# Kernel tuning notes

Hardware: AMD Instinct MI355X
Metric: run time of the kernel (lower is better)

The kernel has to match this reference:

```python
import jax, jax.numpy as jnp
import numpy as np

B, E, D, NH, NP = 4, 32, 1024, 16, 4
LQ = E * E
DH = D // NH


def layer_norm(x, g, b, eps=1e-6):
    m = x.mean(-1, keepdims=True)
    v = ((x - m) ** 2).mean(-1, keepdims=True)
    return (x - m) / jnp.sqrt(v + eps) * g + b


def get_ref(H, W):
    # matches MSCrossAttnBlock.get_reference_points: centers normalized to [0,1], (x, y) order
    ys, xs = jnp.meshgrid((jnp.arange(H, dtype=jnp.float32) + 0.5) / H,
                          (jnp.arange(W, dtype=jnp.float32) + 0.5) / W, indexing='ij')
    return jnp.stack([xs.ravel(), ys.ravel()], -1)  # (H*W, 2)


def bilinear_sample(value_l, loc, H, W):
    # value_l: (N, nH, H*W, dh); loc: (N, Lq, nH, P, 2) normalized to [0,1]
    # replicates F.grid_sample(align_corners=False, padding_mode='zeros') with grid = 2*loc - 1
    N, Lq, nH, P, _ = loc.shape
    x = loc[..., 0] * W - 0.5
    y = loc[..., 1] * H - 0.5
    x0 = jnp.floor(x)
    y0 = jnp.floor(y)
    wx1 = x - x0
    wy1 = y - y0
    out = 0.0
    for dy, wy in ((0, 1.0 - wy1), (1, wy1)):
        for dx, wx in ((0, 1.0 - wx1), (1, wx1)):
            xi = x0 + dx
            yi = y0 + dy
            valid = (xi >= 0) & (xi < W) & (yi >= 0) & (yi < H)
            idx = (jnp.clip(yi, 0, H - 1) * W + jnp.clip(xi, 0, W - 1)).astype(jnp.int32)
            idx_t = idx.transpose(0, 2, 1, 3).reshape(N, nH, Lq * P)  # (N, nH, Lq*P)
            g = jnp.take_along_axis(value_l, idx_t[..., None], axis=2)  # (N, nH, Lq*P, dh)
            g = g.reshape(N, nH, Lq, P, -1).transpose(0, 2, 1, 3, 4)  # (N, Lq, nH, P, dh)
            w = (wx * wy) * valid.astype(value_l.dtype)
            out = out + g * w[..., None]
    return out


def msdeform(query, ref, inp, shapes, Wv, bv, Wo, bo, Wa, ba, Wp, bp):
    # MSDeformAttn forward (no padding mask)
    N, Lq, d = query.shape
    nL = len(shapes)
    value = (inp @ Wv.T + bv).reshape(N, -1, NH, DH).transpose(0, 2, 1, 3)  # (N, nH, Lin, dh)
    off = (query @ Wo.T + bo).reshape(N, Lq, NH, nL, NP, 2)
    attw = jax.nn.softmax((query @ Wa.T + ba).reshape(N, Lq, NH, nL * NP), axis=-1)
    attw = attw.reshape(N, Lq, NH, nL, NP)
    normalizer = jnp.array([[w, h] for (h, w) in shapes], dtype=query.dtype)  # (nL, 2) = [W, H]
    loc = ref[None, :, None, None, None, :] + off / normalizer[None, None, None, :, None, :]
    out = 0.0
    start = 0
    for l, (H, W) in enumerate(shapes):
        sampled = bilinear_sample(value[:, :, start:start + H * W], loc[:, :, :, l], H, W)
        out = out + (sampled * attw[:, :, :, l, :, None]).sum(3)  # (N, Lq, nH, dh)
        start += H * W
    return out.reshape(N, Lq, d) @ Wp.T + bp


def setup_inputs() -> dict:
    key = jax.random.key(0)
    ks = iter(jax.random.split(key, 64))
    def rnd(shape, scale):
        return jax.random.normal(next(ks), shape, dtype=jnp.float32) * scale
    inp = {}
    for i in range(4):
        inp[f'src{i}'] = rnd((B, LQ, D), 1.0)
    for nm in ('qn', 'fn', 'n1'):
        inp[nm + '_g'] = jnp.ones((D,), jnp.float32)
        inp[nm + '_b'] = jnp.zeros((D,), jnp.float32)
    inp['gamma1'] = rnd((D,), 0.1)
    inp['gamma2'] = rnd((D,), 0.1)
    ws = D ** -0.5
    for pre, nl in (('ca', 4), ('sa', 1)):
        inp[pre + '_vw'] = rnd((D, D), ws)
        inp[pre + '_vb'] = jnp.zeros((D,), jnp.float32)
        inp[pre + '_ow'] = rnd((NH * nl * NP * 2, D), ws)
        inp[pre + '_ob'] = rnd((NH * nl * NP * 2,), 0.1)
        inp[pre + '_aw'] = rnd((NH * nl * NP, D), ws)
        inp[pre + '_ab'] = jnp.zeros((NH * nl * NP,), jnp.float32)
        inp[pre + '_pw'] = rnd((D, D), ws)
        inp[pre + '_pb'] = jnp.zeros((D,), jnp.float32)
    return inp


def reference(src0, src1, src2, src3, qn_g, qn_b, fn_g, fn_b, n1_g, n1_b, gamma1, gamma2,
              ca_vw, ca_vb, ca_ow, ca_ob, ca_aw, ca_ab, ca_pw, ca_pb,
              sa_vw, sa_vb, sa_ow, sa_ob, sa_aw, sa_ab, sa_pw, sa_pb):
    shapes4 = [(E, E)] * 4
    feat = jnp.concatenate([src0, src1, src2, src3], axis=1)  # (B, 4*LQ, D)
    query = src3  # srcs[-1], pos embed is None
    ref = get_ref(E, E)  # (LQ, 2)
    attn = msdeform(layer_norm(query, qn_g, qn_b), ref, layer_norm(feat, fn_g, fn_b),
                    shapes4, ca_vw, ca_vb, ca_ow, ca_ob, ca_aw, ca_ab, ca_pw, ca_pb)
    attn1 = layer_norm(attn, n1_g, n1_b)
    attn2 = msdeform(attn1, ref, attn1, [(E, E)],
                     sa_vw, sa_vb, sa_ow, sa_ob, sa_aw, sa_ab, sa_pw, sa_pb)
    attn = attn + gamma2 * attn2
    return query + gamma1 * attn
```

## Files before the change

### kernel.cpp

```cpp
#include <hip/hip_runtime.h>


#define DEV __device__ __forceinline__

typedef float f32x4 __attribute__((ext_vector_type(4)));
typedef __bf16 bf16x8 __attribute__((ext_vector_type(8)));

DEV unsigned short f2bf(float f) {
  union { float f; unsigned u; } a; a.f = f;
  unsigned r = a.u + 0x7fffu + ((a.u >> 16) & 1u);
  return (unsigned short)(r >> 16);
}
DEV float bf2f(unsigned short h) {
  union { unsigned u; float f; } a; a.u = ((unsigned)h) << 16;
  return a.f;
}

DEV void gld16(const unsigned short* g, unsigned short* l) {
  __builtin_amdgcn_global_load_lds(
      (const __attribute__((address_space(1))) void*)g,
      (__attribute__((address_space(3))) void*)l, 16, 0, 0);
}

struct CvtArgs {
  const float* src[8];
  unsigned short* dst;
  int off4[9];
};

__global__ __launch_bounds__(256) void f2bf_multi(CvtArgs a) {
  int i = blockIdx.x * 256 + threadIdx.x;
  int seg = 0;
  #pragma unroll
  for (int s = 1; s < 8; ++s) seg += (i >= a.off4[s]) ? 1 : 0;
  const float4 v = ((const float4*)a.src[seg])[i - a.off4[seg]];
  unsigned short* o = a.dst + (size_t)i * 4;
  o[0] = f2bf(v.x); o[1] = f2bf(v.y); o[2] = f2bf(v.z); o[3] = f2bf(v.w);
}

DEV void ln_row(const float* __restrict__ xr, const float* __restrict__ g,
                const float* __restrict__ b, unsigned short* __restrict__ op_row) {
  float4 v = ((const float4*)xr)[threadIdx.x];
  float s  = v.x + v.y + v.z + v.w;
  float s2 = v.x*v.x + v.y*v.y + v.z*v.z + v.w*v.w;
  #pragma unroll
  for (int o = 32; o; o >>= 1) { s += __shfl_down(s, o); s2 += __shfl_down(s2, o); }
  __shared__ float red[8];
  int wave = threadIdx.x >> 6, lane = threadIdx.x & 63;
  if (lane == 0) { red[wave] = s; red[4 + wave] = s2; }
  __syncthreads();
  if (threadIdx.x == 0) {
    float ts  = red[0] + red[1] + red[2] + red[3];
    float ts2 = red[4] + red[5] + red[6] + red[7];
    float mean = ts * (1.f / 1024.f);
    float var  = ts2 * (1.f / 1024.f) - mean * mean;
    red[0] = mean; red[1] = rsqrtf(var + 1e-6f);
  }
  __syncthreads();
  float mean = red[0], rstd = red[1];
  float4 gg = ((const float4*)g)[threadIdx.x];
  float4 bb = ((const float4*)b)[threadIdx.x];
  unsigned short* op = op_row + threadIdx.x * 4;
  op[0] = f2bf((v.x - mean) * rstd * gg.x + bb.x);
  op[1] = f2bf((v.y - mean) * rstd * gg.y + bb.y);
  op[2] = f2bf((v.z - mean) * rstd * gg.z + bb.z);
  op[3] = f2bf((v.w - mean) * rstd * gg.w + bb.w);
}

__global__ __launch_bounds__(256) void ln_bf16_kernel(
    const float* __restrict__ x, const float* __restrict__ g,
    const float* __restrict__ b, unsigned short* __restrict__ out) {
  int row = blockIdx.x;
  ln_row(x + (size_t)row * 1024, g, b, out + (size_t)row * 1024);
}

__global__ __launch_bounds__(256) void ln4_kernel(
    const float* __restrict__ s0, const float* __restrict__ s1,
    const float* __restrict__ s2, const float* __restrict__ s3,
    const float* __restrict__ g, const float* __restrict__ b,
    unsigned short* __restrict__ out) {
  int blk = blockIdx.x;
  int l = blk >> 12, inner = blk & 4095;
  const float* srcs[4] = {s0, s1, s2, s3};
  int orow = (inner >> 10) * 4096 + l * 1024 + (inner & 1023);
  ln_row(srcs[l] + (size_t)inner * 1024, g, b, out + (size_t)orow * 1024);
}

struct GemmP {
  const unsigned short* A; const unsigned short* W;
  void* C; void* C1; void* C2;
  const float* b0; const float* b1; const float* b2;
  const float* src3; const float* g1; const float* g2; const float* attnp;
  int M, N, K;
};

template <int BM, int BN, int EPI>
__global__ __launch_bounds__(256) void gemm_glds(GemmP P) {
  constexpr int BK = 32;
  constexpr int WMT = BM / 2, WNT = BN / 2;
  constexpr int MF = WMT / 16, NF = WNT / 16;
  constexpr int AG = BM / 16, BG = BN / 16;
  constexpr int PA = AG / 4, PB = BG / 4;
  __shared__ __align__(16) unsigned short sA[BM * BK];
  __shared__ __align__(16) unsigned short sB[BN * BK];
  const int tid = threadIdx.x;
  const int wave = tid >> 6, lane = tid & 63;
  const int wm = (wave & 1) * WMT, wn = (wave >> 1) * WNT;
  const int m0 = blockIdx.x * BM, n0 = blockIdx.y * BN;
  const int lq = lane >> 4, lm = lane & 15;
  const int r16 = lane >> 2;
  const int cst = lane & 3;
  const int csrc = cst ^ ((r16 >> 1) & 3);
  const int aslot = lq ^ ((lm >> 1) & 3);

  f32x4 acc[MF][NF] = {};

  for (int k0 = 0; k0 < P.K; k0 += BK) {
    __syncthreads();
    #pragma unroll
    for (int p = 0; p < PA; ++p) {
      int g = wave + 4 * p;
      int grow = m0 + g * 16 + r16;
      gld16(P.A + (size_t)grow * P.K + k0 + csrc * 8, sA + g * 512);
    }
    #pragma unroll
    for (int p = 0; p < PB; ++p) {
      int g = wave + 4 * p;
      int grow = n0 + g * 16 + r16;
      grow = min(grow, P.N - 1);
      gld16(P.W + (size_t)grow * P.K + k0 + csrc * 8, sB + g * 512);
    }
    __syncthreads();
    bf16x8 af[MF], bfr[NF];
    #pragma unroll
    for (int mi = 0; mi < MF; ++mi)
      af[mi] = *(const bf16x8*)(sA + ((wm >> 4) + mi) * 512 + lm * 32 + aslot * 8);
    #pragma unroll
    for (int ni = 0; ni < NF; ++ni)
      bfr[ni] = *(const bf16x8*)(sB + ((wn >> 4) + ni) * 512 + lm * 32 + aslot * 8);
    #pragma unroll
    for (int mi = 0; mi < MF; ++mi)
      #pragma unroll
      for (int ni = 0; ni < NF; ++ni)
        acc[mi][ni] = __builtin_amdgcn_mfma_f32_16x16x32_bf16(
            af[mi], bfr[ni], acc[mi][ni], 0, 0, 0);
  }

  #pragma unroll
  for (int mi = 0; mi < MF; ++mi) {
    #pragma unroll
    for (int ni = 0; ni < NF; ++ni) {
      const int col = n0 + wn + ni * 16 + lm;
      #pragma unroll
      for (int r2 = 0; r2 < 4; ++r2) {
        const int row = m0 + wm + mi * 16 + lq * 4 + r2;
        float v = acc[mi][ni][r2];
        if constexpr (EPI == 0) {
          ((float*)P.C)[(size_t)row * 1024 + col] = v + P.b0[col];
        } else if constexpr (EPI == 1) {
          ((unsigned short*)P.C)[(size_t)row * 1024 + col] = f2bf(v + P.b0[col]);
        } else if constexpr (EPI == 2) {
          if (col < 512)
            ((float*)P.C)[(size_t)row * 512 + col] = v + P.b0[col];
          else
            ((float*)P.C1)[(size_t)row * 256 + col - 512] = v + P.b1[col - 512];
        } else if constexpr (EPI == 3) {
          if (col < 1024)
            ((unsigned short*)P.C)[(size_t)row * 1024 + col] = f2bf(v + P.b0[col]);
          else if (col < 1152)
            ((float*)P.C1)[(size_t)row * 128 + col - 1024] = v + P.b1[col - 1024];
          else if (col < 1216)
            ((float*)P.C2)[(size_t)row * 64 + col - 1152] = v + P.b2[col - 1152];
        } else {
          size_t i = (size_t)row * 1024 + col;
          float vv = v + P.b0[col];
          ((float*)P.C)[i] = P.src3[i] + P.g1[col] * (P.attnp[i] + P.g2[col] * vv);
        }
      }
    }
  }
}

template <int NLEV>
__global__ __launch_bounds__(256) void ms_sample_fused(
    const unsigned short* __restrict__ value, const float* __restrict__ off,
    const float* __restrict__ logits, unsigned short* __restrict__ out) {
  const int nq = blockIdx.x;
  const int wave = threadIdx.x >> 6, lane = threadIdx.x & 63;
  const int h = (wave << 2) + (lane >> 4);
  const int c = (lane & 15) << 2;
  const int q = nq & 1023, n = nq >> 10;
  const float* offp = off + ((size_t)nq * 16 + h) * (NLEV * 8);
  const float* lgp  = logits + ((size_t)nq * 16 + h) * (NLEV * 4);

  float lg[NLEV * 4];
  #pragma unroll
  for (int i = 0; i < NLEV; ++i) {
    float4 v = ((const float4*)lgp)[i];
    lg[4*i] = v.x; lg[4*i+1] = v.y; lg[4*i+2] = v.z; lg[4*i+3] = v.w;
  }
  float mx = lg[0];
  #pragma unroll
  for (int i = 1; i < NLEV * 4; ++i) mx = fmaxf(mx, lg[i]);
  float ssum = 0.f;
  #pragma unroll
  for (int i = 0; i < NLEV * 4; ++i) { lg[i] = __expf(lg[i] - mx); ssum += lg[i]; }
  const float inv = 1.f / ssum;

  const float fqx = (float)(q & 31), fqy = (float)(q >> 5);
  float a0 = 0.f, a1 = 0.f, a2 = 0.f, a3 = 0.f;

  #pragma unroll
  for (int l = 0; l < NLEV; ++l) {
    const unsigned short* vl =
        value + ((size_t)(n * NLEV + l) << 20) + h * 64 + c;
    #pragma unroll
    for (int p = 0; p < 4; ++p) {
      float2 o2 = ((const float2*)offp)[l * 4 + p];
      float aw = lg[l * 4 + p] * inv;
      float xx = fqx + o2.x, yy = fqy + o2.y;
      float xf = floorf(xx), yf = floorf(yy);
      float fx = xx - xf, fy = yy - yf;
      int ix = (int)xf, iy = (int)yf;
      int ix1 = ix + 1, iy1 = iy + 1;
      float vx0 = ((unsigned)ix  < 32u) ? 1.f : 0.f;
      float vx1 = ((unsigned)ix1 < 32u) ? 1.f : 0.f;
      float vy0 = ((unsigned)iy  < 32u) ? 1.f : 0.f;
      float vy1 = ((unsigned)iy1 < 32u) ? 1.f : 0.f;
      int cx0 = min(max(ix, 0), 31), cx1 = min(max(ix1, 0), 31);
      int cy0 = min(max(iy, 0), 31), cy1 = min(max(iy1, 0), 31);
      float w00 = (1.f - fx) * (1.f - fy) * vx0 * vy0 * aw;
      float w01 = fx * (1.f - fy) * vx1 * vy0 * aw;
      float w10 = (1.f - fx) * fy * vx0 * vy1 * aw;
      float w11 = fx * fy * vx1 * vy1 * aw;
      ushort4 u00 = *(const ushort4*)(vl + ((size_t)(cy0 * 32 + cx0) << 10));
      ushort4 u01 = *(const ushort4*)(vl + ((size_t)(cy0 * 32 + cx1) << 10));
      ushort4 u10 = *(const ushort4*)(vl + ((size_t)(cy1 * 32 + cx0) << 10));
      ushort4 u11 = *(const ushort4*)(vl + ((size_t)(cy1 * 32 + cx1) << 10));
      a0 += w00 * bf2f(u00.x) + w01 * bf2f(u01.x) + w10 * bf2f(u10.x) + w11 * bf2f(u11.x);
      a1 += w00 * bf2f(u00.y) + w01 * bf2f(u01.y) + w10 * bf2f(u10.y) + w11 * bf2f(u11.y);
      a2 += w00 * bf2f(u00.z) + w01 * bf2f(u01.z) + w10 * bf2f(u10.z) + w11 * bf2f(u11.z);
      a3 += w00 * bf2f(u00.w) + w01 * bf2f(u01.w) + w10 * bf2f(u10.w) + w11 * bf2f(u11.w);
    }
  }
  ushort4 r;
  r.x = f2bf(a0); r.y = f2bf(a1); r.z = f2bf(a2); r.w = f2bf(a3);
  *(ushort4*)(out + ((size_t)nq * 16 + h) * 64 + c) = r;
}

extern "C" void kernel_launch(void* const* d_in, const int* in_sizes, int n_in,
                              void* d_out, int out_size, void* d_ws,
                              size_t ws_size, hipStream_t stream) {
  (void)in_sizes; (void)n_in; (void)out_size; (void)ws_size;
  const float* src[4] = {(const float*)d_in[0], (const float*)d_in[1],
                         (const float*)d_in[2], (const float*)d_in[3]};
  const float* qn_g = (const float*)d_in[4];
  const float* qn_b = (const float*)d_in[5];
  const float* fn_g = (const float*)d_in[6];
  const float* fn_b = (const float*)d_in[7];
  const float* n1_g = (const float*)d_in[8];
  const float* n1_b = (const float*)d_in[9];
  const float* gamma1 = (const float*)d_in[10];
  const float* gamma2 = (const float*)d_in[11];
  const float* ca_vw = (const float*)d_in[12];
  const float* ca_vb = (const float*)d_in[13];
  const float* ca_ow = (const float*)d_in[14];
  const float* ca_ob = (const float*)d_in[15];
  const float* ca_aw = (const float*)d_in[16];
  const float* ca_ab = (const float*)d_in[17];
  const float* ca_pw = (const float*)d_in[18];
  const float* ca_pb = (const float*)d_in[19];
  const float* sa_vw = (const float*)d_in[20];
  const float* sa_vb = (const float*)d_in[21];
  const float* sa_ow = (const float*)d_in[22];
  const float* sa_ob = (const float*)d_in[23];
  const float* sa_aw = (const float*)d_in[24];
  const float* sa_ab = (const float*)d_in[25];
  const float* sa_pw = (const float*)d_in[26];
  const float* sa_pb = (const float*)d_in[27];

  char* wsp = (char*)d_ws;
  size_t off = 0;
  auto alloc = [&](size_t bytes) {
    char* r = wsp + off;
    off = (off + bytes + 255) & ~(size_t)255;
    return r;
  };
  const size_t MB = 1024 * 1024;
  unsigned short* w_ca_vw = (unsigned short*)alloc(1024 * 1024 * 2);
  unsigned short* w_ca_ow = (unsigned short*)alloc(512 * 1024 * 2);
  unsigned short* w_ca_aw = (unsigned short*)alloc(256 * 1024 * 2);
  unsigned short* w_ca_pw = (unsigned short*)alloc(1024 * 1024 * 2);
  unsigned short* w_sa_vw = (unsigned short*)alloc(1024 * 1024 * 2);
  unsigned short* w_sa_ow = (unsigned short*)alloc(128 * 1024 * 2);
  unsigned short* w_sa_aw = (unsigned short*)alloc(64 * 1024 * 2);
  unsigned short* w_sa_pw = (unsigned short*)alloc(1024 * 1024 * 2);
  (void)w_ca_aw; (void)w_sa_ow; (void)w_sa_aw;
  char* R1 = alloc(32 * MB);
  char* R2 = alloc(32 * MB);
  char* R3 = alloc(8 * MB);
  char* R4 = alloc(8 * MB);
  char* R5 = alloc(4 * MB);

  unsigned short* f_ln    = (unsigned short*)R1;
  float*          attn    = (float*)R1;
  unsigned short* attn1   = (unsigned short*)(R1 + 16 * MB);
  unsigned short* samp_sa = (unsigned short*)(R1 + 24 * MB);
  unsigned short* val_ca  = (unsigned short*)R2;
  unsigned short* val_sa  = (unsigned short*)R2;
  unsigned short* q_ln    = (unsigned short*)R3;
  unsigned short* samp_ca = (unsigned short*)R3;
  float*          off_ca  = (float*)R4;
  float*          off_sa  = (float*)R4;
  float*          attw_sa = (float*)(R4 + 4 * MB);
  float*          attw_ca = (float*)R5;

  CvtArgs ca;
  ca.src[0] = ca_vw; ca.src[1] = ca_ow; ca.src[2] = ca_aw; ca.src[3] = ca_pw;
  ca.src[4] = sa_vw; ca.src[5] = sa_ow; ca.src[6] = sa_aw; ca.src[7] = sa_pw;
  ca.dst = w_ca_vw;
  const int sizes4[8] = {262144, 131072, 65536, 262144, 262144, 32768, 16384, 262144};
  ca.off4[0] = 0;
  for (int i = 0; i < 8; ++i) ca.off4[i + 1] = ca.off4[i] + sizes4[i];
  f2bf_multi<<<ca.off4[8] / 256, 256, 0, stream>>>(ca);

  ln_bf16_kernel<<<4096, 256, 0, stream>>>(src[3], qn_g, qn_b, q_ln);
  ln4_kernel<<<16384, 256, 0, stream>>>(src[0], src[1], src[2], src[3],
                                        fn_g, fn_b, f_ln);

  auto mkP = [](const unsigned short* A, const unsigned short* W, void* C,
                const float* b0, int M, int N, int K) {
    GemmP p{}; p.A = A; p.W = W; p.C = C; p.b0 = b0; p.M = M; p.N = N; p.K = K;
    return p;
  };

  gemm_glds<128, 128, 1><<<dim3(128, 8), 256, 0, stream>>>(
      mkP(f_ln, w_ca_vw, val_ca, ca_vb, 16384, 1024, 1024));
  {
    GemmP p = mkP(q_ln, w_ca_ow, off_ca, ca_ob, 4096, 768, 1024);
    p.C1 = attw_ca; p.b1 = ca_ab;
    gemm_glds<128, 128, 2><<<dim3(32, 6), 256, 0, stream>>>(p);
  }

  ms_sample_fused<4><<<4096, 256, 0, stream>>>(val_ca, off_ca, attw_ca, samp_ca);
  gemm_glds<64, 128, 0><<<dim3(64, 8), 256, 0, stream>>>(
      mkP(samp_ca, w_ca_pw, attn, ca_pb, 4096, 1024, 1024));

  ln_bf16_kernel<<<4096, 256, 0, stream>>>(attn, n1_g, n1_b, attn1);
  {
    GemmP p = mkP(attn1, w_sa_vw, val_sa, sa_vb, 4096, 1216, 1024);
    p.C1 = off_sa; p.b1 = sa_ob; p.C2 = attw_sa; p.b2 = sa_ab;
    gemm_glds<128, 128, 3><<<dim3(32, 10), 256, 0, stream>>>(p);
  }
  ms_sample_fused<1><<<4096, 256, 0, stream>>>(val_sa, off_sa, attw_sa, samp_sa);
  {
    GemmP p = mkP(samp_sa, w_sa_pw, d_out, sa_pb, 4096, 1024, 1024);
    p.src3 = src[3]; p.g1 = gamma1; p.g2 = gamma2; p.attnp = attn;
    gemm_glds<64, 128, 4><<<dim3(64, 8), 256, 0, stream>>>(p);
  }
}
```

Measured before the change: 415.5 us.

## Rework GEMM to register-staged BK=64 loads, 1D grid, smaller tiles, fused LN

The GEMM drops the global_load_lds direct-to-LDS path. It now loads two 32-wide K slabs into registers, stores them to LDS, and runs MFMA over both, so each iteration covers a K step of 64 and needs fewer barriers. The grid becomes 1D with M as the fastest-varying tile index for better weight reuse across neighbouring blocks. The offset/attention and self-attention value GEMMs switch to 64x128 tiles to raise block counts. The query LayerNorm is folded into the feature LayerNorm launch. Costs: more registers per thread and doubled LDS per block, which may reduce occupancy, and the loads now pass through VGPRs instead of going straight to LDS.

```diff
diff --git a/kernel.cpp b/kernel.cpp
--- a/kernel.cpp
+++ b/kernel.cpp
@@ -14,12 +14,6 @@
 DEV float bf2f(unsigned short h) {
   union { unsigned u; float f; } a; a.u = ((unsigned)h) << 16;
   return a.f;
-}
-
-DEV void gld16(const unsigned short* g, unsigned short* l) {
-  __builtin_amdgcn_global_load_lds(
-      (const __attribute__((address_space(1))) void*)g,
-      (__attribute__((address_space(3))) void*)l, 16, 0, 0);
 }
 
 struct CvtArgs {
@@ -74,16 +68,22 @@
   ln_row(x + (size_t)row * 1024, g, b, out + (size_t)row * 1024);
 }
 
-__global__ __launch_bounds__(256) void ln4_kernel(
+__global__ __launch_bounds__(256) void ln5_kernel(
     const float* __restrict__ s0, const float* __restrict__ s1,
     const float* __restrict__ s2, const float* __restrict__ s3,
-    const float* __restrict__ g, const float* __restrict__ b,
-    unsigned short* __restrict__ out) {
+    const float* __restrict__ fg, const float* __restrict__ fb,
+    const float* __restrict__ qg, const float* __restrict__ qb,
+    unsigned short* __restrict__ f_out, unsigned short* __restrict__ q_out) {
   int blk = blockIdx.x;
-  int l = blk >> 12, inner = blk & 4095;
-  const float* srcs[4] = {s0, s1, s2, s3};
-  int orow = (inner >> 10) * 4096 + l * 1024 + (inner & 1023);
-  ln_row(srcs[l] + (size_t)inner * 1024, g, b, out + (size_t)orow * 1024);
+  int seg = blk >> 12, inner = blk & 4095;
+  if (seg < 4) {
+    const float* srcs[4] = {s0, s1, s2, s3};
+    int orow = (inner >> 10) * 4096 + seg * 1024 + (inner & 1023);
+    ln_row(srcs[seg] + (size_t)inner * 1024, fg, fb,
+           f_out + (size_t)orow * 1024);
+  } else {
+    ln_row(s3 + (size_t)inner * 1024, qg, qb, q_out + (size_t)inner * 1024);
+  }
 }
 
 struct GemmP {
@@ -91,22 +91,22 @@
   void* C; void* C1; void* C2;
   const float* b0; const float* b1; const float* b2;
   const float* src3; const float* g1; const float* g2; const float* attnp;
-  int M, N, K;
+  int M, N, K, tilesM;
 };
 
 template <int BM, int BN, int EPI>
-__global__ __launch_bounds__(256) void gemm_glds(GemmP P) {
-  constexpr int BK = 32;
+__global__ __launch_bounds__(256) void gemm_v3(GemmP P) {
   constexpr int WMT = BM / 2, WNT = BN / 2;
   constexpr int MF = WMT / 16, NF = WNT / 16;
-  constexpr int AG = BM / 16, BG = BN / 16;
-  constexpr int PA = AG / 4, PB = BG / 4;
-  __shared__ __align__(16) unsigned short sA[BM * BK];
-  __shared__ __align__(16) unsigned short sB[BN * BK];
+  constexpr int PA = BM / 64, PB = BN / 64;
+  __shared__ __align__(16) unsigned short sA[BM * 64];
+  __shared__ __align__(16) unsigned short sB[BN * 64];
   const int tid = threadIdx.x;
   const int wave = tid >> 6, lane = tid & 63;
   const int wm = (wave & 1) * WMT, wn = (wave >> 1) * WNT;
-  const int m0 = blockIdx.x * BM, n0 = blockIdx.y * BN;
+  const int id = blockIdx.x;
+  const int m0 = (id % P.tilesM) * BM;
+  const int n0 = (id / P.tilesM) * BN;
   const int lq = lane >> 4, lm = lane & 15;
   const int r16 = lane >> 2;
   const int cst = lane & 3;
@@ -114,36 +114,50 @@
   const int aslot = lq ^ ((lm >> 1) & 3);
 
   f32x4 acc[MF][NF] = {};
-
-  for (int k0 = 0; k0 < P.K; k0 += BK) {
+  bf16x8 ald[2][PA], bld[2][PB];
+
+  #pragma unroll 1
+  for (int k0 = 0; k0 < P.K; k0 += 64) {
+    #pragma unroll
+    for (int s = 0; s < 2; ++s) {
+      #pragma unroll
+      for (int p = 0; p < PA; ++p) {
+        int grow = m0 + (wave + 4 * p) * 16 + r16;
+        ald[s][p] = *(const bf16x8*)(P.A + (size_t)grow * P.K + k0 + s * 32 + csrc * 8);
+      }
+      #pragma unroll
+      for (int p = 0; p < PB; ++p) {
+        int grow = min(n0 + (wave + 4 * p) * 16 + r16, P.N - 1);
+        bld[s][p] = *(const bf16x8*)(P.W + (size_t)grow * P.K + k0 + s * 32 + csrc * 8);
+      }
+    }
     __syncthreads();
     #pragma unroll
-    for (int p = 0; p < PA; ++p) {
-      int g = wave + 4 * p;
-      int grow = m0 + g * 16 + r16;
-      gld16(P.A + (size_t)grow * P.K + k0 + csrc * 8, sA + g * 512);
-    }
-    #pragma unroll
-    for (int p = 0; p < PB; ++p) {
-      int g = wave + 4 * p;
-      int grow = n0 + g * 16 + r16;
-      grow = min(grow, P.N - 1);
-      gld16(P.W + (size_t)grow * P.K + k0 + csrc * 8, sB + g * 512);
+    for (int s = 0; s < 2; ++s) {
+      #pragma unroll
+      for (int p = 0; p < PA; ++p)
+        *(bf16x8*)(sA + s * BM * 32 + (wave + 4 * p) * 512 + (r16 * 4 + cst) * 8) = ald[s][p];
+      #pragma unroll
+      for (int p = 0; p < PB; ++p)
+        *(bf16x8*)(sB + s * BN * 32 + (wave + 4 * p) * 512 + (r16 * 4 + cst) * 8) = bld[s][p];
     }
     __syncthreads();
-    bf16x8 af[MF], bfr[NF];
-    #pragma unroll
-    for (int mi = 0; mi < MF; ++mi)
-      af[mi] = *(const bf16x8*)(sA + ((wm >> 4) + mi) * 512 + lm * 32 + aslot * 8);
-    #pragma unroll
-    for (int ni = 0; ni < NF; ++ni)
-      bfr[ni] = *(const bf16x8*)(sB + ((wn >> 4) + ni) * 512 + lm * 32 + aslot * 8);
-    #pragma unroll
-    for (int mi = 0; mi < MF; ++mi)
+    #pragma unroll
+    for (int s = 0; s < 2; ++s) {
+      bf16x8 af[MF], bfr[NF];
+      #pragma unroll
+      for (int mi = 0; mi < MF; ++mi)
+        af[mi] = *(const bf16x8*)(sA + s * BM * 32 + ((wm >> 4) + mi) * 512 + lm * 32 + aslot * 8);
       #pragma unroll
       for (int ni = 0; ni < NF; ++ni)
-        acc[mi][ni] = __builtin_amdgcn_mfma_f32_16x16x32_bf16(
-            af[mi], bfr[ni], acc[mi][ni], 0, 0, 0);
+        bfr[ni] = *(const bf16x8*)(sB + s * BN * 32 + ((wn >> 4) + ni) * 512 + lm * 32 + aslot * 8);
+      #pragma unroll
+      for (int mi = 0; mi < MF; ++mi)
+        #pragma unroll
+        for (int ni = 0; ni < NF; ++ni)
+          acc[mi][ni] = __builtin_amdgcn_mfma_f32_16x16x32_bf16(
+              af[mi], bfr[ni], acc[mi][ni], 0, 0, 0);
+    }
   }
 
   #pragma unroll
@@ -324,38 +338,38 @@
   for (int i = 0; i < 8; ++i) ca.off4[i + 1] = ca.off4[i] + sizes4[i];
   f2bf_multi<<<ca.off4[8] / 256, 256, 0, stream>>>(ca);
 
-  ln_bf16_kernel<<<4096, 256, 0, stream>>>(src[3], qn_g, qn_b, q_ln);
-  ln4_kernel<<<16384, 256, 0, stream>>>(src[0], src[1], src[2], src[3],
-                                        fn_g, fn_b, f_ln);
+  ln5_kernel<<<20480, 256, 0, stream>>>(src[0], src[1], src[2], src[3],
+                                        fn_g, fn_b, qn_g, qn_b, f_ln, q_ln);
 
   auto mkP = [](const unsigned short* A, const unsigned short* W, void* C,
-                const float* b0, int M, int N, int K) {
-    GemmP p{}; p.A = A; p.W = W; p.C = C; p.b0 = b0; p.M = M; p.N = N; p.K = K;
+                const float* b0, int M, int N, int K, int tilesM) {
+    GemmP p{}; p.A = A; p.W = W; p.C = C; p.b0 = b0;
+    p.M = M; p.N = N; p.K = K; p.tilesM = tilesM;
     return p;
   };
 
-  gemm_glds<128, 128, 1><<<dim3(128, 8), 256, 0, stream>>>(
-      mkP(f_ln, w_ca_vw, val_ca, ca_vb, 16384, 1024, 1024));
+  gemm_v3<128, 128, 1><<<128 * 8, 256, 0, stream>>>(
+      mkP(f_ln, w_ca_vw, val_ca, ca_vb, 16384, 1024, 1024, 128));
   {
-    GemmP p = mkP(q_ln, w_ca_ow, off_ca, ca_ob, 4096, 768, 1024);
+    GemmP p = mkP(q_ln, w_ca_ow, off_ca, ca_ob, 4096, 768, 1024, 64);
     p.C1 = attw_ca; p.b1 = ca_ab;
-    gemm_glds<128, 128, 2><<<dim3(32, 6), 256, 0, stream>>>(p);
+    gemm_v3<64, 128, 2><<<64 * 6, 256, 0, stream>>>(p);
   }
 
   ms_sample_fused<4><<<4096, 256, 0, stream>>>(val_ca, off_ca, attw_ca, samp_ca);
-  gemm_glds<64, 128, 0><<<dim3(64, 8), 256, 0, stream>>>(
-      mkP(samp_ca, w_ca_pw, attn, ca_pb, 4096, 1024, 1024));
+  gemm_v3<64, 128, 0><<<64 * 8, 256, 0, stream>>>(
+      mkP(samp_ca, w_ca_pw, attn, ca_pb, 4096, 1024, 1024, 64));
 
   ln_bf16_kernel<<<4096, 256, 0, stream>>>(attn, n1_g, n1_b, attn1);
   {
-    GemmP p = mkP(attn1, w_sa_vw, val_sa, sa_vb, 4096, 1216, 1024);
+    GemmP p = mkP(attn1, w_sa_vw, val_sa, sa_vb, 4096, 1216, 1024, 64);
     p.C1 = off_sa; p.b1 = sa_ob; p.C2 = attw_sa; p.b2 = sa_ab;
-    gemm_glds<128, 128, 3><<<dim3(32, 10), 256, 0, stream>>>(p);
+    gemm_v3<64, 128, 3><<<64 * 10, 256, 0, stream>>>(p);
   }
   ms_sample_fused<1><<<4096, 256, 0, stream>>>(val_sa, off_sa, attw_sa, samp_sa);
   {
-    GemmP p = mkP(samp_sa, w_sa_pw, d_out, sa_pb, 4096, 1024, 1024);
+    GemmP p = mkP(samp_sa, w_sa_pw, d_out, sa_pb, 4096, 1024, 1024, 64);
     p.src3 = src[3]; p.g1 = gamma1; p.g2 = gamma2; p.attnp = attn;
-    gemm_glds<64, 128, 4><<<dim3(64, 8), 256, 0, stream>>>(p);
-  }
-}
+    gemm_v3<64, 128, 4><<<64 * 8, 256, 0, stream>>>(p);
+  }
+}
```

Measured after the change: 366.6 us. 11.8% less time.
